# Optimization experiments

Measured on AMD Instinct MI355X. Metric: run time of the kernel, lower is better.

Reference implementation:

```python
import jax, jax.numpy as jnp
import numpy as np

MARGIN = 0.3
NEG_FILL = 1000000.0


def setup_inputs() -> dict:
    key = jax.random.key(0)
    k1, k2 = jax.random.split(key)
    features = jax.random.normal(k1, (8192, 128), dtype=jnp.float32)
    labels = jax.random.randint(k2, (8192,), 0, 512, dtype=jnp.int64)
    return {"features": features, "labels": labels}


def _triplet_loss(features, labels):
    N = features.shape[0]
    # pairwise euclidean distances via gram trick (matches torch.cdist p=2)
    sq = jnp.sum(features * features, axis=1)               # [N]
    d2 = sq[:, None] + sq[None, :] - 2.0 * (features @ features.T)
    d2 = jnp.maximum(d2, 0.0)
    # guard sqrt(0) on diagonal for clean gradients
    dist = jnp.where(d2 > 0.0, jnp.sqrt(jnp.where(d2 > 0.0, d2, 1.0)), 0.0)  # [N,N]

    same = labels[:, None] == labels[None, :]
    eye = jnp.eye(N, dtype=bool)
    is_pos = same & ~eye
    is_neg = ~same

    neg_inf = jnp.float32(-jnp.inf)
    pos_inf = jnp.float32(jnp.inf)
    has_pos = jnp.any(is_pos, axis=1)
    has_neg = jnp.any(is_neg, axis=1)
    # hardest positive: masked row max; empty -> 0.0
    dist_ap = jnp.max(jnp.where(is_pos, dist, neg_inf), axis=1)
    dist_ap = jnp.where(has_pos, dist_ap, 0.0)
    # hardest negative: masked row min; empty -> 1e6
    dist_an = jnp.min(jnp.where(is_neg, dist, pos_inf), axis=1)
    dist_an = jnp.where(has_neg, dist_an, NEG_FILL)

    # MarginRankingLoss with y=1: mean(max(0, margin - (dist_an - dist_ap)))
    return jnp.mean(jnp.maximum(0.0, MARGIN - (dist_an - dist_ap)))


def reference(features, labels):
    return _triplet_loss(features, labels)
```

## Files before the change

### kernel.cpp

```cpp
#include <hip/hip_runtime.h>
#include <hip/hip_bf16.h>
#include <math.h>

#define N 8192
#define D 128
#define MARGIN_V 0.3f
#define NEG_FILL 1000000.0f

typedef short bf16x8 __attribute__((ext_vector_type(8)));
typedef float f32x4  __attribute__((ext_vector_type(4)));

__device__ __forceinline__ void g2l16(const void* g, void* l) {
    __builtin_amdgcn_global_load_lds(
        (const __attribute__((address_space(1))) void*)g,
        (__attribute__((address_space(3))) void*)l, 16, 0, 0);
}

__global__ __launch_bounds__(256) void convert_kernel(const float* __restrict__ F,
                                                      unsigned short* __restrict__ Fb,
                                                      float* __restrict__ sq,
                                                      unsigned* __restrict__ ap,
                                                      unsigned* __restrict__ an) {
    int row  = blockIdx.x * 4 + (threadIdx.x >> 6);
    int lane = threadIdx.x & 63;
    float2 v = *(const float2*)&F[row * D + lane * 2];
    float s = v.x * v.x + v.y * v.y;
    __hip_bfloat162 t = __float22bfloat162_rn(v);
    *(unsigned int*)&Fb[row * D + lane * 2] = *(unsigned int*)&t;
    #pragma unroll
    for (int off = 32; off >= 1; off >>= 1) s += __shfl_xor(s, off);
    if (lane == 0) sq[row] = s;
    int gid = blockIdx.x * 256 + threadIdx.x;
    if (gid < N) { ap[gid] = 0u; an[gid] = 0x7F800000u; }
}

__global__ __launch_bounds__(256, 2) void gemm_kernel(const unsigned short* __restrict__ Fb,
                                                      const float* __restrict__ sq,
                                                      const int* __restrict__ lab,
                                                      unsigned* __restrict__ ap,
                                                      unsigned* __restrict__ an) {
    __shared__ __align__(16) unsigned short As[128 * 128];
    __shared__ float sqj_s[1024];
    __shared__ int   labj_s[1024];
    __shared__ float sqi_s[128];
    __shared__ int   labi_s[128];

    const int bi = blockIdx.x & 63;
    const int jc = blockIdx.x >> 6;
    const int i0 = bi * 128;
    const int jbase0 = jc * 1024;
    const int tid  = threadIdx.x;
    const int wave = tid >> 6, lane = tid & 63;
    const int wy = wave >> 1, wx = wave & 1;
    const int quad = lane >> 4, lr = lane & 15;

    {
        f32x4 v = *(const f32x4*)&sq[jbase0 + tid * 4];
        *(f32x4*)&sqj_s[tid * 4] = v;
        int4 w4 = *(const int4*)&lab[jbase0 + tid * 4];
        *(int4*)&labj_s[tid * 4] = w4;
    }
    if (tid < 128) { sqi_s[tid] = sq[i0 + tid]; labi_s[tid] = lab[i0 + tid]; }

    #pragma unroll
    for (int it = 0; it < 8; ++it) {
        int c_id = it * 256 + tid;
        int row = c_id >> 4, p = c_id & 15;
        int sc = (p & 8) | ((p ^ row) & 7);
        g2l16(Fb + (size_t)(i0 + row) * D + sc * 8, (char*)As + c_id * 16);
    }
    __syncthreads();

    bf16x8 af[4][4];
    #pragma unroll
    for (int a = 0; a < 4; ++a)
        #pragma unroll
        for (int ks = 0; ks < 4; ++ks) {
            int row = wy * 64 + a * 16 + lr;
            int kc  = ks * 4 + quad;
            int pos = (kc & 8) | ((kc ^ row) & 7);
            af[a][ks] = *(const bf16x8*)&As[row * 128 + pos * 8];
        }
    f32x4 sqi4[4]; int4 labi4[4];
    #pragma unroll
    for (int a = 0; a < 4; ++a) {
        int base = wy * 64 + a * 16 + quad * 4;
        sqi4[a]  = *(const f32x4*)&sqi_s[base];
        labi4[a] = *(const int4*)&labi_s[base];
    }

    float rowP[4][4], rowN[4][4];
    #pragma unroll
    for (int a = 0; a < 4; ++a)
        #pragma unroll
        for (int r = 0; r < 4; ++r) { rowP[a][r] = -INFINITY; rowN[a][r] = INFINITY; }

    const unsigned short* Bp = Fb + (size_t)(jbase0 + wx * 32 + lr) * D + quad * 8;
    const int c0 = wx * 32 + lr;

#define LOAD_BTILE(T, DST)                                                      \
    {                                                                           \
        _Pragma("unroll")                                                       \
        for (int b = 0; b < 2; ++b) {                                           \
            const unsigned short* p_ = Bp + (size_t)((T) * 64 + b * 16) * D;    \
            _Pragma("unroll")                                                   \
            for (int ks = 0; ks < 4; ++ks)                                      \
                DST[b][ks] = *(const bf16x8*)(p_ + ks * 32);                    \
        }                                                                       \
    }

#define COMPUTE_TILE(T, BFR)                                                    \
    {                                                                           \
        float sqj_l[2]; int labj_l[2];                                          \
        _Pragma("unroll")                                                       \
        for (int b = 0; b < 2; ++b) {                                           \
            int cl = (T) * 64 + c0 + b * 16;                                    \
            sqj_l[b]  = sqj_s[cl];                                              \
            labj_l[b] = labj_s[cl];                                             \
        }                                                                       \
        f32x4 acc[4][2];                                                        \
        _Pragma("unroll")                                                       \
        for (int a = 0; a < 4; ++a)                                             \
            _Pragma("unroll")                                                   \
            for (int b = 0; b < 2; ++b) acc[a][b] = {0.f, 0.f, 0.f, 0.f};       \
        _Pragma("unroll")                                                       \
        for (int ks = 0; ks < 4; ++ks)                                          \
            _Pragma("unroll")                                                   \
            for (int a = 0; a < 4; ++a)                                         \
                _Pragma("unroll")                                               \
                for (int b = 0; b < 2; ++b)                                     \
                    acc[a][b] = __builtin_amdgcn_mfma_f32_16x16x32_bf16(        \
                        af[a][ks], BFR[b][ks], acc[a][b], 0, 0, 0);             \
        _Pragma("unroll")                                                       \
        for (int a = 0; a < 4; ++a)                                             \
            _Pragma("unroll")                                                   \
            for (int b = 0; b < 2; ++b)                                         \
                _Pragma("unroll")                                               \
                for (int r = 0; r < 4; ++r) {                                   \
                    float u = fmaf(acc[a][b][r], -2.0f, sqj_l[b]);              \
                    bool same = (labi4[a][r] == labj_l[b]);                     \
                    rowP[a][r] = fmaxf(rowP[a][r], same ? u : -INFINITY);       \
                    rowN[a][r] = fminf(rowN[a][r], same ? INFINITY : u);        \
                }                                                               \
    }

    bf16x8 bf0[2][4], bf1[2][4];
    LOAD_BTILE(0, bf0);
    #pragma unroll 1
    for (int t = 0; t < 16; t += 2) {
        LOAD_BTILE(t + 1, bf1);
        COMPUTE_TILE(t, bf0);
        if (t + 2 < 16) LOAD_BTILE(t + 2, bf0);
        COMPUTE_TILE(t + 1, bf1);
    }
#undef LOAD_BTILE
#undef COMPUTE_TILE

    #pragma unroll
    for (int a = 0; a < 4; ++a)
        #pragma unroll
        for (int r = 0; r < 4; ++r) {
            float p = rowP[a][r], n = rowN[a][r];
            #pragma unroll
            for (int off = 1; off < 16; off <<= 1) {
                p = fmaxf(p, __shfl_xor(p, off));
                n = fminf(n, __shfl_xor(n, off));
            }
            rowP[a][r] = p; rowN[a][r] = n;
        }
    if (lr == 0) {
        #pragma unroll
        for (int a = 0; a < 4; ++a)
            #pragma unroll
            for (int r = 0; r < 4; ++r) {
                int row = i0 + wy * 64 + a * 16 + quad * 4 + r;
                float pd2 = fmaxf(sqi4[a][r] + rowP[a][r], 0.f);
                float nd2 = fmaxf(sqi4[a][r] + rowN[a][r], 0.f);
                atomicMax(&ap[row], __float_as_uint(pd2));
                atomicMin(&an[row], __float_as_uint(nd2));
            }
    }
}

__global__ __launch_bounds__(256) void loss_kernel(const float* __restrict__ ap,
                                                   const float* __restrict__ an,
                                                   float* __restrict__ out) {
    int tid = threadIdx.x;
    float sum = 0.f;
    #pragma unroll
    for (int k = 0; k < 8; ++k) {
        int i = k * 1024 + tid * 4;
        f32x4 a4 = *(const f32x4*)&ap[i];
        f32x4 n4 = *(const f32x4*)&an[i];
        #pragma unroll
        for (int c = 0; c < 4; ++c) {
            float apd = __builtin_amdgcn_sqrtf(a4[c]);
            float anv = n4[c];
            float and_ = (anv < INFINITY) ? __builtin_amdgcn_sqrtf(anv) : NEG_FILL;
            sum += fmaxf(0.f, MARGIN_V - (and_ - apd));
        }
    }
    #pragma unroll
    for (int off = 32; off >= 1; off >>= 1) sum += __shfl_xor(sum, off);
    __shared__ float s4[4];
    if ((tid & 63) == 0) s4[tid >> 6] = sum;
    __syncthreads();
    if (tid == 0) out[0] = (s4[0] + s4[1] + s4[2] + s4[3]) * (1.0f / (float)N);
}

extern "C" void kernel_launch(void* const* d_in, const int* in_sizes, int n_in,
                              void* d_out, int out_size, void* d_ws, size_t ws_size,
                              hipStream_t stream) {
    const float* F   = (const float*)d_in[0];
    const int*   lab = (const int*)d_in[1];

    unsigned short* Fb = (unsigned short*)d_ws;
    float*          sq = (float*)(Fb + (size_t)N * D);
    unsigned*       ap = (unsigned*)(sq + N);
    unsigned*       an = ap + N;

    convert_kernel<<<N / 4, 256, 0, stream>>>(F, Fb, sq, ap, an);
    gemm_kernel<<<512, 256, 0, stream>>>(Fb, sq, lab, ap, an);
    loss_kernel<<<1, 256, 0, stream>>>((const float*)ap, (const float*)an, (float*)d_out);
}
```

Before: 94.71 us.

## Pre-swizzle bf16 features into MFMA fragment layout and drop LDS staging

The convert kernel now writes the bf16 features in a layout matching the MFMA operand fragments, so each lane's 16-byte load is contiguous and fully coalesced. The gemm kernel drops shared-memory staging of the A tile, sq and labels, loading fragments and per-column metadata straight from global memory. Each block now covers 256 rows by 512 columns instead of 128 rows by 1024 columns. This removes LDS traffic and a barrier, at the cost of more scattered small global loads for sq and labels and more reliance on cache for B reuse.

```diff
diff --git a/kernel.cpp b/kernel.cpp
--- a/kernel.cpp
+++ b/kernel.cpp
@@ -10,27 +10,41 @@
 typedef short bf16x8 __attribute__((ext_vector_type(8)));
 typedef float f32x4  __attribute__((ext_vector_type(4)));
 
-__device__ __forceinline__ void g2l16(const void* g, void* l) {
-    __builtin_amdgcn_global_load_lds(
-        (const __attribute__((address_space(1))) void*)g,
-        (__attribute__((address_space(3))) void*)l, 16, 0, 0);
-}
 
 __global__ __launch_bounds__(256) void convert_kernel(const float* __restrict__ F,
                                                       unsigned short* __restrict__ Fb,
                                                       float* __restrict__ sq,
                                                       unsigned* __restrict__ ap,
                                                       unsigned* __restrict__ an) {
-    int row  = blockIdx.x * 4 + (threadIdx.x >> 6);
-    int lane = threadIdx.x & 63;
-    float2 v = *(const float2*)&F[row * D + lane * 2];
-    float s = v.x * v.x + v.y * v.y;
-    __hip_bfloat162 t = __float22bfloat162_rn(v);
-    *(unsigned int*)&Fb[row * D + lane * 2] = *(unsigned int*)&t;
-    #pragma unroll
-    for (int off = 32; off >= 1; off >>= 1) s += __shfl_xor(s, off);
-    if (lane == 0) sq[row] = s;
-    int gid = blockIdx.x * 256 + threadIdx.x;
+    __shared__ float red[16][17];
+    const int g   = blockIdx.x;
+    const int tid = threadIdx.x;
+    const int q = tid >> 6, L = tid & 63;
+    const int m = L & 15, j8 = (L >> 4) * 8;
+
+    const float* src = F + (size_t)(16 * g + m) * D + 32 * q + j8;
+    float4 v0 = *(const float4*)src;
+    float4 v1 = *(const float4*)(src + 4);
+
+    float s = v0.x * v0.x + v0.y * v0.y + v0.z * v0.z + v0.w * v0.w
+            + v1.x * v1.x + v1.y * v1.y + v1.z * v1.z + v1.w * v1.w;
+
+    union { bf16x8 v; __hip_bfloat162 h2[4]; } pk;
+    pk.h2[0] = __float22bfloat162_rn({v0.x, v0.y});
+    pk.h2[1] = __float22bfloat162_rn({v0.z, v0.w});
+    pk.h2[2] = __float22bfloat162_rn({v1.x, v1.y});
+    pk.h2[3] = __float22bfloat162_rn({v1.z, v1.w});
+    *(bf16x8*)&Fb[(size_t)g * 2048 + tid * 8] = pk.v;
+
+    red[m][q * 4 + (L >> 4)] = s;
+    __syncthreads();
+    if (tid < 16) {
+        float t = 0.f;
+        #pragma unroll
+        for (int c = 0; c < 16; ++c) t += red[tid][c];
+        sq[16 * g + tid] = t;
+    }
+    int gid = blockIdx.x * 256 + tid;
     if (gid < N) { ap[gid] = 0u; an[gid] = 0x7F800000u; }
 }
 
@@ -39,54 +53,29 @@
                                                       const int* __restrict__ lab,
                                                       unsigned* __restrict__ ap,
                                                       unsigned* __restrict__ an) {
-    __shared__ __align__(16) unsigned short As[128 * 128];
-    __shared__ float sqj_s[1024];
-    __shared__ int   labj_s[1024];
-    __shared__ float sqi_s[128];
-    __shared__ int   labi_s[128];
-
-    const int bi = blockIdx.x & 63;
-    const int jc = blockIdx.x >> 6;
-    const int i0 = bi * 128;
-    const int jbase0 = jc * 1024;
     const int tid  = threadIdx.x;
     const int wave = tid >> 6, lane = tid & 63;
-    const int wy = wave >> 1, wx = wave & 1;
     const int quad = lane >> 4, lr = lane & 15;
-
-    {
-        f32x4 v = *(const f32x4*)&sq[jbase0 + tid * 4];
-        *(f32x4*)&sqj_s[tid * 4] = v;
-        int4 w4 = *(const int4*)&lab[jbase0 + tid * 4];
-        *(int4*)&labj_s[tid * 4] = w4;
-    }
-    if (tid < 128) { sqi_s[tid] = sq[i0 + tid]; labi_s[tid] = lab[i0 + tid]; }
-
-    #pragma unroll
-    for (int it = 0; it < 8; ++it) {
-        int c_id = it * 256 + tid;
-        int row = c_id >> 4, p = c_id & 15;
-        int sc = (p & 8) | ((p ^ row) & 7);
-        g2l16(Fb + (size_t)(i0 + row) * D + sc * 8, (char*)As + c_id * 16);
-    }
-    __syncthreads();
+    const int S = blockIdx.x >> 4;
+    const int C = blockIdx.x & 15;
+    const int R0   = S * 256 + wave * 64;
+    const int g0   = R0 >> 4;
+    const int cg0  = C * 32;
+    const int colb = C * 512;
 
     bf16x8 af[4][4];
     #pragma unroll
     for (int a = 0; a < 4; ++a)
         #pragma unroll
-        for (int ks = 0; ks < 4; ++ks) {
-            int row = wy * 64 + a * 16 + lr;
-            int kc  = ks * 4 + quad;
-            int pos = (kc & 8) | ((kc ^ row) & 7);
-            af[a][ks] = *(const bf16x8*)&As[row * 128 + pos * 8];
-        }
+        for (int ks = 0; ks < 4; ++ks)
+            af[a][ks] = *(const bf16x8*)&Fb[(((size_t)(g0 + a) * 4 + ks) * 64 + lane) * 8];
+
     f32x4 sqi4[4]; int4 labi4[4];
     #pragma unroll
     for (int a = 0; a < 4; ++a) {
-        int base = wy * 64 + a * 16 + quad * 4;
-        sqi4[a]  = *(const f32x4*)&sqi_s[base];
-        labi4[a] = *(const int4*)&labi_s[base];
+        int base = R0 + a * 16 + quad * 4;
+        sqi4[a]  = *(const f32x4*)&sq[base];
+        labi4[a] = *(const int4*)&lab[base];
     }
 
     float rowP[4][4], rowN[4][4];
@@ -95,66 +84,60 @@
         #pragma unroll
         for (int r = 0; r < 4; ++r) { rowP[a][r] = -INFINITY; rowN[a][r] = INFINITY; }
 
-    const unsigned short* Bp = Fb + (size_t)(jbase0 + wx * 32 + lr) * D + quad * 8;
-    const int c0 = wx * 32 + lr;
-
-#define LOAD_BTILE(T, DST)                                                      \
-    {                                                                           \
-        _Pragma("unroll")                                                       \
-        for (int b = 0; b < 2; ++b) {                                           \
-            const unsigned short* p_ = Bp + (size_t)((T) * 64 + b * 16) * D;    \
-            _Pragma("unroll")                                                   \
-            for (int ks = 0; ks < 4; ++ks)                                      \
-                DST[b][ks] = *(const bf16x8*)(p_ + ks * 32);                    \
-        }                                                                       \
-    }
-
-#define COMPUTE_TILE(T, BFR)                                                    \
-    {                                                                           \
-        float sqj_l[2]; int labj_l[2];                                          \
-        _Pragma("unroll")                                                       \
-        for (int b = 0; b < 2; ++b) {                                           \
-            int cl = (T) * 64 + c0 + b * 16;                                    \
-            sqj_l[b]  = sqj_s[cl];                                              \
-            labj_l[b] = labj_s[cl];                                             \
-        }                                                                       \
-        f32x4 acc[4][2];                                                        \
-        _Pragma("unroll")                                                       \
-        for (int a = 0; a < 4; ++a)                                             \
-            _Pragma("unroll")                                                   \
-            for (int b = 0; b < 2; ++b) acc[a][b] = {0.f, 0.f, 0.f, 0.f};       \
-        _Pragma("unroll")                                                       \
-        for (int ks = 0; ks < 4; ++ks)                                          \
-            _Pragma("unroll")                                                   \
-            for (int a = 0; a < 4; ++a)                                         \
-                _Pragma("unroll")                                               \
-                for (int b = 0; b < 2; ++b)                                     \
-                    acc[a][b] = __builtin_amdgcn_mfma_f32_16x16x32_bf16(        \
-                        af[a][ks], BFR[b][ks], acc[a][b], 0, 0, 0);             \
-        _Pragma("unroll")                                                       \
-        for (int a = 0; a < 4; ++a)                                             \
-            _Pragma("unroll")                                                   \
-            for (int b = 0; b < 2; ++b)                                         \
-                _Pragma("unroll")                                               \
-                for (int r = 0; r < 4; ++r) {                                   \
-                    float u = fmaf(acc[a][b][r], -2.0f, sqj_l[b]);              \
-                    bool same = (labi4[a][r] == labj_l[b]);                     \
-                    rowP[a][r] = fmaxf(rowP[a][r], same ? u : -INFINITY);       \
-                    rowN[a][r] = fminf(rowN[a][r], same ? INFINITY : u);        \
-                }                                                               \
-    }
-
-    bf16x8 bf0[2][4], bf1[2][4];
-    LOAD_BTILE(0, bf0);
+#define LOADT(T, BF, SQJ, LABJ)                                                   \
+    {                                                                             \
+        _Pragma("unroll")                                                         \
+        for (int b = 0; b < 2; ++b) {                                             \
+            int gb = cg0 + 2 * (T) + b;                                           \
+            _Pragma("unroll")                                                     \
+            for (int ks = 0; ks < 4; ++ks)                                        \
+                BF[b][ks] = *(const bf16x8*)&Fb[(((size_t)gb * 4 + ks) * 64 + lane) * 8]; \
+            SQJ[b]  = sq[colb + (T) * 32 + b * 16 + lr];                          \
+            LABJ[b] = lab[colb + (T) * 32 + b * 16 + lr];                         \
+        }                                                                         \
+    }
+
+#define COMP(BF, SQJ, LABJ)                                                       \
+    {                                                                             \
+        f32x4 acc[4][2];                                                          \
+        _Pragma("unroll")                                                         \
+        for (int a = 0; a < 4; ++a)                                               \
+            _Pragma("unroll")                                                     \
+            for (int b = 0; b < 2; ++b) acc[a][b] = {0.f, 0.f, 0.f, 0.f};         \
+        _Pragma("unroll")                                                         \
+        for (int ks = 0; ks < 4; ++ks)                                            \
+            _Pragma("unroll")                                                     \
+            for (int a = 0; a < 4; ++a)                                           \
+                _Pragma("unroll")                                                 \
+                for (int b = 0; b < 2; ++b)                                       \
+                    acc[a][b] = __builtin_amdgcn_mfma_f32_16x16x32_bf16(          \
+                        af[a][ks], BF[b][ks], acc[a][b], 0, 0, 0);                \
+        _Pragma("unroll")                                                         \
+        for (int a = 0; a < 4; ++a)                                               \
+            _Pragma("unroll")                                                     \
+            for (int b = 0; b < 2; ++b)                                           \
+                _Pragma("unroll")                                                 \
+                for (int r = 0; r < 4; ++r) {                                     \
+                    float u = fmaf(acc[a][b][r], -2.0f, SQJ[b]);                  \
+                    bool same = (labi4[a][r] == LABJ[b]);                         \
+                    rowP[a][r] = fmaxf(rowP[a][r], same ? u : -INFINITY);         \
+                    rowN[a][r] = fminf(rowN[a][r], same ? INFINITY : u);          \
+                }                                                                 \
+    }
+
+    bf16x8 b0[2][4], b1[2][4];
+    float sq0[2], sq1[2];
+    int   lb0[2], lb1[2];
+    LOADT(0, b0, sq0, lb0);
     #pragma unroll 1
     for (int t = 0; t < 16; t += 2) {
-        LOAD_BTILE(t + 1, bf1);
-        COMPUTE_TILE(t, bf0);
-        if (t + 2 < 16) LOAD_BTILE(t + 2, bf0);
-        COMPUTE_TILE(t + 1, bf1);
-    }
-#undef LOAD_BTILE
-#undef COMPUTE_TILE
+        LOADT(t + 1, b1, sq1, lb1);
+        COMP(b0, sq0, lb0);
+        if (t + 2 < 16) LOADT(t + 2, b0, sq0, lb0);
+        COMP(b1, sq1, lb1);
+    }
+#undef LOADT
+#undef COMP
 
     #pragma unroll
     for (int a = 0; a < 4; ++a)
@@ -173,7 +156,7 @@
         for (int a = 0; a < 4; ++a)
             #pragma unroll
             for (int r = 0; r < 4; ++r) {
-                int row = i0 + wy * 64 + a * 16 + quad * 4 + r;
+                int row = R0 + a * 16 + quad * 4 + r;
                 float pd2 = fmaxf(sqi4[a][r] + rowP[a][r], 0.f);
                 float nd2 = fmaxf(sqi4[a][r] + rowN[a][r], 0.f);
                 atomicMax(&ap[row], __float_as_uint(pd2));
@@ -219,7 +202,7 @@
     unsigned*       ap = (unsigned*)(sq + N);
     unsigned*       an = ap + N;
 
-    convert_kernel<<<N / 4, 256, 0, stream>>>(F, Fb, sq, ap, an);
+    convert_kernel<<<N / 16, 256, 0, stream>>>(F, Fb, sq, ap, an);
     gemm_kernel<<<512, 256, 0, stream>>>(Fb, sq, lab, ap, an);
     loss_kernel<<<1, 256, 0, stream>>>((const float*)ap, (const float*)an, (float*)d_out);
 }
```

New measurement: 85.88 us. 1.1x faster.
